# Performance work log

Hardware: AMD Instinct MI355X
Metric: run time of the kernel (lower is better)

Reference implementation:

```python
import jax, jax.numpy as jnp
import numpy as np

B, L, H, NH, NE, M = 4, 1024, 768, 12, 42, 8
EMB = 768
OFFSET = 1  # bert cls offset


def setup_inputs() -> dict:
    key = jax.random.key(0)
    ks = jax.random.split(key, 6)
    seq = jax.random.normal(ks[0], (B, L, H), jnp.float32)
    attn = jax.random.uniform(ks[1], (B, NH, L, L), jnp.float32)
    attn = attn / attn.sum(-1, keepdims=True)  # row-stochastic like softmaxed attention probs
    W_head = jax.random.normal(ks[2], (2 * H, EMB), jnp.float32) * 0.02
    b_head = jnp.zeros((EMB,), jnp.float32)
    W_tail = jax.random.normal(ks[3], (2 * H, EMB), jnp.float32) * 0.02
    b_tail = jnp.zeros((EMB,), jnp.float32)
    # mention start positions (before +offset); keep start+offset < L
    mention_pos = jax.random.randint(ks[4], (B, NE, M), 0, L - OFFSET - 1)
    counts = jax.random.randint(ks[5], (B, NE), 1, M + 1)  # >=1 valid mention per entity
    mention_mask = jnp.arange(M)[None, None, :] < counts[:, :, None]
    return dict(sequence_output=seq, attention=attn, W_head=W_head, b_head=b_head,
                W_tail=W_tail, b_tail=b_tail, mention_pos=mention_pos,
                mention_mask=mention_mask)


def _get_hrt(seq, attn, mention_pos, mention_mask):
    # seq: [B,L,H]; attn: [B,NH,L,L]; mention_pos/mask: [B,NE,M]
    b_idx = jnp.arange(B)[:, None, None]
    pos = mention_pos + OFFSET                          # [B,NE,M]
    m_emb = seq[b_idx, pos]                             # [B,NE,M,H] mention embeddings
    att_t = jnp.transpose(attn, (0, 2, 1, 3))           # [B,L,NH,L]
    m_att = att_t[b_idx, pos]                           # [B,NE,M,NH,L] mention attentions
    mask = mention_mask
    neg_inf = jnp.finfo(seq.dtype).min
    # per-entity logsumexp pooling over mentions
    ent_emb = jax.nn.logsumexp(jnp.where(mask[..., None], m_emb, neg_inf), axis=2)
    has_m = mask.any(axis=2)
    ent_emb = jnp.where(has_m[..., None], ent_emb, 0.0)  # [B,NE,H]
    cnt = mask.sum(axis=2).astype(seq.dtype)
    ent_att = (m_att * mask[..., None, None].astype(seq.dtype)).sum(axis=2)
    ent_att = ent_att / jnp.maximum(cnt, 1.0)[..., None, None]  # [B,NE,NH,L] mean over mentions
    # all ordered (head, tail) pairs on the NE x NE grid
    hs = jnp.broadcast_to(ent_emb[:, :, None, :], (B, NE, NE, H))
    ts = jnp.broadcast_to(ent_emb[:, None, :, :], (B, NE, NE, H))
    # ht_att = relu(mean_h(h_att * t_att)), normalized over seq, then context = ht_att @ seq
    ht = jnp.einsum('bihl,bjhl->bijl', ent_att, ent_att) / NH  # [B,NE,NE,L]
    ht = jax.nn.relu(ht)
    ht = ht / (ht.sum(-1, keepdims=True) + 1e-10)
    rs = jnp.einsum('bijl,bld->bijd', ht, seq)                  # [B,NE,NE,H]
    return hs, rs, ts


def reference(sequence_output, attention, W_head, b_head, W_tail, b_tail, mention_pos, mention_mask):
    hs, rs, ts = _get_hrt(sequence_output, attention, mention_pos, mention_mask)
    h_out = jnp.tanh(jnp.concatenate([hs, rs], axis=-1) @ W_head + b_head)
    t_out = jnp.tanh(jnp.concatenate([ts, rs], axis=-1) @ W_tail + b_tail)
    return h_out, t_out
```

## Files before the change

kernel.cpp:

```cpp
#include <hip/hip_runtime.h>
#include <math.h>

typedef _Float16 f16;
typedef __attribute__((ext_vector_type(4))) _Float16 f16x4;
typedef __attribute__((ext_vector_type(8))) _Float16 f16x8;
typedef __attribute__((ext_vector_type(4))) float f32x4;

#define B_    4
#define L_    1024
#define H_    768
#define NH_   12
#define NE_   42
#define M_    8
#define E2_   1536
#define HTP_  1792
#define OUT_HALF 5419008LL

typedef __attribute__((address_space(1))) const unsigned char ga_t;
typedef __attribute__((address_space(3))) unsigned char la_t;
__device__ __forceinline__ void async16(const void* g, void* l) {
    __builtin_amdgcn_global_load_lds((ga_t*)g, (la_t*)l, 16, 0, 0);
}

__device__ __forceinline__ float fast_tanh(float x) {
    float e = __expf(2.f * x);
    return 1.f - 2.f / (e + 1.f);
}


__device__ void prep_body(int bid, char* smem,
                          const float* __restrict__ Wh, const float* __restrict__ Wt,
                          const float* __restrict__ bh, const float* __restrict__ bt,
                          f16* __restrict__ wtop, f16* __restrict__ wbot,
                          float* __restrict__ bcat) {
    float (*tile)[33] = (float(*)[33])smem;
    int tx = bid % 24, ty = (bid / 24) % 24, m = bid / 576;
    const float* src = (m & 1) ? Wt : Wh;
    int roff = (m & 2) ? H_ : 0;
    f16* dst = (m & 2) ? wbot : wtop;
    int coff = (m & 1) ? H_ : 0;
    int x = threadIdx.x & 31, y8 = threadIdx.x >> 5;
#pragma unroll
    for (int r = 0; r < 4; r++) {
        int h = ty*32 + y8 + r*8, c = tx*32 + x;
        tile[y8 + r*8][x] = src[(long long)(roff + h)*H_ + c];
    }
    __syncthreads();
#pragma unroll
    for (int r = 0; r < 4; r++) {
        int c2 = tx*32 + y8 + r*8, h2 = ty*32 + x;
        dst[(long long)(coff + c2)*H_ + h2] = (f16)tile[x][y8 + r*8];
    }
    if (bid == 0) {
        for (int idx = threadIdx.x; idx < E2_; idx += 256)
            bcat[idx] = (idx < H_) ? bh[idx] : bt[idx - H_];
    }
}

__device__ void seq16_body(int bid, const float* __restrict__ seq,
                           f16* __restrict__ seq16) {
    int idx = (bid*256 + threadIdx.x) * 4;
    f32x4 v = *(const f32x4*)(seq + idx);
    f16x4 o = {(f16)v[0], (f16)v[1], (f16)v[2], (f16)v[3]};
    *(f16x4*)(seq16 + idx) = o;
}

__device__ void ent_emb_body(int bid, const float* __restrict__ seq,
                             const int* __restrict__ mpos,
                             const int* __restrict__ mmask,
                             f16* __restrict__ ent) {
    int e = bid % NE_, b = bid / NE_;
    int tid = threadIdx.x;
    const int* mp = mpos  + (b*NE_ + e)*M_;
    const int* mk = mmask + (b*NE_ + e)*M_;
    int pos[M_], msk[M_];
#pragma unroll
    for (int m = 0; m < M_; m++) { msk[m] = mk[m]; pos[m] = mp[m] + 1; }
#pragma unroll
    for (int q = 0; q < 3; q++) {
        int h = tid + q*256;
        float mx = -1e30f, vals[M_];
#pragma unroll
        for (int m = 0; m < M_; m++) {
            vals[m] = 0.f;
            if (msk[m]) {
                float v = seq[((long long)b*L_ + pos[m])*H_ + h];
                vals[m] = v; mx = fmaxf(mx, v);
            }
        }
        float s = 0.f;
#pragma unroll
        for (int m = 0; m < M_; m++) if (msk[m]) s += __expf(vals[m] - mx);
        float lse = (mx > -1e29f) ? mx + __logf(s) : 0.f;
        ent[(b*NE_ + e)*H_ + h] = (f16)lse;
    }
}

__device__ void ent_att_body(int bid, const float* __restrict__ attn,
                             const int* __restrict__ mpos,
                             const int* __restrict__ mmask,
                             f16* __restrict__ eatt) {
    int nh = bid % NH_, e = (bid / NH_) % NE_, b = bid / (NH_*NE_);
    int tid = threadIdx.x;
    int l0 = tid * 4;
    const int* mp = mpos  + (b*NE_ + e)*M_;
    const int* mk = mmask + (b*NE_ + e)*M_;
    const float* abase = attn + (long long)(b*NH_ + nh) * L_ * L_;
    f32x4 acc = {0,0,0,0}; int cnt = 0;
#pragma unroll
    for (int m = 0; m < M_; m++) {
        if (mk[m]) {
            cnt++;
            const float* row = abase + (long long)(mp[m] + 1) * L_;
            acc += *(const f32x4*)(row + l0);
        }
    }
    float inv = 1.f / (float)(cnt > 0 ? cnt : 1);
    f16x4 o = {(f16)(acc[0]*inv), (f16)(acc[1]*inv), (f16)(acc[2]*inv), (f16)(acc[3]*inv)};
    *(f16x4*)(eatt + ((long long)(b*NE_ + e)*NH_ + nh)*L_ + l0) = o;
}

__device__ void ht_body(int bid, char* smem, const f16* __restrict__ eatt,
                        f16* __restrict__ HT) {
    int jg = bid % 6, i = (bid / 6) % NE_, b = bid / 252;
    int tid = threadIdx.x;
    f16* ei_s = (f16*)smem;
    float (*red)[4] = (float(*)[4])(smem + NH_*L_*2);
    const f16* ei = eatt + (long long)(b*NE_ + i)*NH_*L_;
#pragma unroll
    for (int q = 0; q < 6; q++) {
        int off = (q*256 + tid)*8;
        *(f16x8*)(ei_s + off) = *(const f16x8*)(ei + off);
    }
    __syncthreads();
    int l0 = tid*4;
    int wave = tid >> 6, lane = tid & 63;
    for (int jj = 0; jj < 7; jj++) {
        int j = jg*7 + jj;
        const f16* ej = eatt + (long long)(b*NE_ + j)*NH_*L_;
        f32x4 acc = {0,0,0,0};
#pragma unroll
        for (int h = 0; h < NH_; h++) {
            f16x4 vi = *(const f16x4*)(ei_s + h*L_ + l0);
            f16x4 vj = *(const f16x4*)(ej   + h*L_ + l0);
#pragma unroll
            for (int r = 0; r < 4; r++) acc[r] += (float)vi[r] * (float)vj[r];
        }
        float v[4]; float s = 0.f;
#pragma unroll
        for (int r = 0; r < 4; r++) {
            float t = acc[r] * (1.f/12.f);
            t = t > 0.f ? t : 0.f;
            v[r] = t; s += t;
        }
#pragma unroll
        for (int m = 1; m < 64; m <<= 1) s += __shfl_xor(s, m, 64);
        if (lane == 0) red[jj][wave] = s;
        __syncthreads();
        float S = red[jj][0] + red[jj][1] + red[jj][2] + red[jj][3];
        float sc = 1.f / (S + 1e-10f);
        f16x4 o = {(f16)(v[0]*sc), (f16)(v[1]*sc), (f16)(v[2]*sc), (f16)(v[3]*sc)};
        *(f16x4*)(HT + ((long long)b*HTP_ + i*NE_ + j)*L_ + l0) = o;
    }
}

#define LDSS 40
__device__ void gemm_het_body(int bx, int by, char* smem,
                              const f16* __restrict__ A, const f16* __restrict__ BT,
                              float* __restrict__ het, const float* __restrict__ bcat) {
    const int M = 168, K = 768;
    f16* As = (f16*)smem;
    f16* Bs = (f16*)(smem + 64*LDSS*2);
    int bm = bx*64, bn = by*64;
    int tid = threadIdx.x;
    int wave = tid >> 6, lane = tid & 63;
    int wm = (wave >> 1)*32, wn = (wave & 1)*32;
    int lo4 = lane & 15, kq = (lane >> 4)*8;
    int srow = tid >> 2, scol = (tid & 3)*8;
    bool aval = (bm + srow) < M;
    const f16* aptr = A + (long long)(bm + srow)*K + scol;
    const f16* bptr = BT + (long long)(bn + srow)*K + scol;
    f32x4 acc[2][2] = {};
    for (int k0 = 0; k0 < K; k0 += 32) {
        uint4 zero = {0,0,0,0};
        uint4 av = aval ? *(const uint4*)(aptr + k0) : zero;
        uint4 bv = *(const uint4*)(bptr + k0);
        __syncthreads();
        *(uint4*)(As + srow*LDSS + scol) = av;
        *(uint4*)(Bs + srow*LDSS + scol) = bv;
        __syncthreads();
        f16x8 a0 = *(const f16x8*)(As + (wm +      lo4)*LDSS + kq);
        f16x8 a1 = *(const f16x8*)(As + (wm + 16 + lo4)*LDSS + kq);
        f16x8 b0 = *(const f16x8*)(Bs + (wn +      lo4)*LDSS + kq);
        f16x8 b1 = *(const f16x8*)(Bs + (wn + 16 + lo4)*LDSS + kq);
        acc[0][0] = __builtin_amdgcn_mfma_f32_16x16x32_f16(a0, b0, acc[0][0], 0,0,0);
        acc[0][1] = __builtin_amdgcn_mfma_f32_16x16x32_f16(a0, b1, acc[0][1], 0,0,0);
        acc[1][0] = __builtin_amdgcn_mfma_f32_16x16x32_f16(a1, b0, acc[1][0], 0,0,0);
        acc[1][1] = __builtin_amdgcn_mfma_f32_16x16x32_f16(a1, b1, acc[1][1], 0,0,0);
    }
    int rloc = (lane >> 4)*4;
#pragma unroll
    for (int sm = 0; sm < 2; sm++)
#pragma unroll
    for (int sn = 0; sn < 2; sn++) {
        f32x4 a = acc[sm][sn];
        int c  = bn + wn + sn*16 + lo4;
        int rb = bm + wm + sm*16 + rloc;
#pragma unroll
        for (int r = 0; r < 4; r++)
            if (rb + r < M) het[(rb + r)*E2_ + c] = a[r] + bcat[c];
    }
}

#define LDST 72
template<int MODE>
__device__ void gemm2_body(int bx, int by, int bz, char* smem,
                           const f16* __restrict__ A, const f16* __restrict__ BT, int K,
                           long long strideA, long long strideBT,
                           const float* __restrict__ het, float* __restrict__ outp,
                           f16* __restrict__ outp16) {
    f16* As = (f16*)smem;
    f16* Bs = (f16*)(smem + 8192);
    int bm = bx*128, bn = by*128;
    const f16* Ab = A + strideA*bz;
    const f16* Bb = BT + strideBT*bz;
    int tid = threadIdx.x, wave = tid >> 6, lane = tid & 63;
    int wm = (wave >> 1)*64, wn = (wave & 1)*64;
    int lo4 = lane & 15, kq = (lane >> 4)*8;
    int lrow = lane >> 2, lcol = (lane & 3)*8;
    const f16* ag = Ab + (long long)(bm + wave*32 + lrow)*K + lcol;
    const f16* bg = Bb + (long long)(bn + wave*32 + lrow)*K + lcol;
    f16* asl = As + wave*1024;
    f16* bsl = Bs + wave*1024;
    f32x4 acc[4][4] = {};
    for (int k0 = 0; k0 < K; k0 += 32) {
        async16(ag + k0,          asl);
        async16(ag + k0 + 16*K,   asl + 512);
        async16(bg + k0,          bsl);
        async16(bg + k0 + 16*K,   bsl + 512);
        __syncthreads();
        f16x8 af[4], bf[4];
#pragma unroll
        for (int s = 0; s < 4; s++) {
            af[s] = *(const f16x8*)(As + (wm + s*16 + lo4)*32 + kq);
            bf[s] = *(const f16x8*)(Bs + (wn + s*16 + lo4)*32 + kq);
        }
#pragma unroll
        for (int sm = 0; sm < 4; sm++)
#pragma unroll
        for (int sn = 0; sn < 4; sn++)
            acc[sm][sn] = __builtin_amdgcn_mfma_f32_16x16x32_f16(af[sm], bf[sn], acc[sm][sn], 0,0,0);
        __syncthreads();
    }
    int rloc = (lane >> 4)*4;
    if constexpr (MODE == 1) {
        f16* Ts = (f16*)smem;
        int h_of_wave = wave >> 1;
#pragma unroll
        for (int h = 0; h < 2; h++) {
            if (h_of_wave == h) {
#pragma unroll
                for (int sm = 0; sm < 4; sm++)
#pragma unroll
                for (int sn = 0; sn < 4; sn++) {
                    f32x4 a = acc[sm][sn];
                    int cl = wn + sn*16 + lo4;
                    int ll = sm*16 + rloc;
#pragma unroll
                    for (int r = 0; r < 4; r++)
                        Ts[cl*LDST + ll + r] = (f16)a[r];
                }
            }
            __syncthreads();
            {
                int cl = tid >> 1;
                int lb = (tid & 1)*32;
                f16* dst = outp16 + (long long)bz*E2_*L_
                         + (long long)(bn + cl)*L_ + bm + h*64 + lb;
                const f16* srcl = Ts + cl*LDST + lb;
#pragma unroll
                for (int q = 0; q < 4; q++)
                    *(f16x8*)(dst + q*8) = *(const f16x8*)(srcl + q*8);
            }
            __syncthreads();
        }
    } else {
#pragma unroll
        for (int sm = 0; sm < 4; sm++)
#pragma unroll
        for (int sn = 0; sn < 4; sn++) {
            f32x4 a = acc[sm][sn];
            int c  = bn + wn + sn*16 + lo4;
            int rb = bm + wm + sm*16 + rloc;
#pragma unroll
            for (int r = 0; r < 4; r++) {
                int row = rb + r;
                if (row < NE_*NE_) {
                    int i = row / NE_;
                    int j = row - i*NE_;
                    int sel = (c < H_) ? i : j;
                    float bias = het[(bz*NE_ + sel)*E2_ + c];
                    float v = fast_tanh(a[r] + bias);
                    long long o = (c < H_)
                        ? ((long long)((bz*NE_ + i)*NE_ + j))*H_ + c
                        : OUT_HALF + ((long long)((bz*NE_ + i)*NE_ + j))*H_ + (c - H_);
                    outp[o] = v;
                }
            }
        }
    }
}

__global__ __launch_bounds__(256) void k_L1(
        const float* __restrict__ seq, const float* __restrict__ attn,
        const float* __restrict__ Wh, const float* __restrict__ bh,
        const float* __restrict__ Wt, const float* __restrict__ bt,
        const int* __restrict__ mpos, const int* __restrict__ mmask,
        f16* __restrict__ wtop, f16* __restrict__ wbot, float* __restrict__ bcat,
        f16* __restrict__ seq16, f16* __restrict__ ent, f16* __restrict__ eatt) {
    __shared__ __align__(16) char smem[4224];
    int bid = blockIdx.x;
    if (bid < 2304)       prep_body(bid, smem, Wh, Wt, bh, bt, wtop, wbot, bcat);
    else if (bid < 5376)  seq16_body(bid - 2304, seq, seq16);
    else if (bid < 5544)  ent_emb_body(bid - 5376, seq, mpos, mmask, ent);
    else                  ent_att_body(bid - 5544, attn, mpos, mmask, eatt);
}

__global__ __launch_bounds__(256) void k_L2(
        const f16* __restrict__ seq16, const f16* __restrict__ wbot,
        const f16* __restrict__ ent, const f16* __restrict__ wtop,
        const float* __restrict__ bcat, const f16* __restrict__ eatt,
        f16* __restrict__ seqWT, float* __restrict__ het, f16* __restrict__ HT) {
    __shared__ __align__(16) char smem[24704];
    int bid = blockIdx.x;
    if (bid < 384) {
        int bx = bid & 7, by = (bid >> 3) % 12, bz = bid / 96;
        gemm2_body<1>(bx, by, bz, smem, seq16, wbot, 768,
                      (long long)L_*H_, 0, nullptr, nullptr, seqWT);
    } else if (bid < 1392) {
        ht_body(bid - 384, smem, eatt, HT);
    } else {
        int r = bid - 1392;
        gemm_het_body(r % 3, r / 3, smem, ent, wtop, het, bcat);
    }
}

__global__ __launch_bounds__(256) void k_L3(
        const f16* __restrict__ HT, const f16* __restrict__ seqWT,
        const float* __restrict__ het, float* __restrict__ outp) {
    __shared__ __align__(16) char smem[16384];
    int orig = blockIdx.x;
    int lid  = (orig & 7) * 84 + (orig >> 3);
    int bz   = lid / 168;
    int rem  = lid - bz*168;
    int bx   = rem / 12;
    int by   = rem - bx*12;
    gemm2_body<2>(bx, by, bz, smem, HT, seqWT, 1024,
                  (long long)HTP_*L_, (long long)E2_*L_, het, outp, nullptr);
}

extern "C" void kernel_launch(void* const* d_in, const int* in_sizes, int n_in,
                              void* d_out, int out_size, void* d_ws, size_t ws_size,
                              hipStream_t stream) {
    const float* seq  = (const float*)d_in[0];
    const float* attn = (const float*)d_in[1];
    const float* Wh   = (const float*)d_in[2];
    const float* bh   = (const float*)d_in[3];
    const float* Wt   = (const float*)d_in[4];
    const float* bt   = (const float*)d_in[5];
    const int* mpos   = (const int*)d_in[6];
    const int* mmask  = (const int*)d_in[7];
    float* out = (float*)d_out;
    char* ws = (char*)d_ws;
    f16*   ent   = (f16*)  (ws + 0);
    f16*   wtop  = (f16*)  (ws + 258048);
    f16*   wbot  = (f16*)  (ws + 2617344);
    float* bcat  = (float*)(ws + 4976640);
    float* het   = (float*)(ws + 4982784);
    f16*   eatt  = (f16*)  (ws + 6014976);
    f16*   seq16 = (f16*)  (ws + 10143744);
    f16*   HT    = (f16*)  (ws + 16435200);
    f16*   seqWT = (f16*)  (ws + 31115264);

    k_L1<<<7560, 256, 0, stream>>>(seq, attn, Wh, bh, Wt, bt, mpos, mmask,
                                   wtop, wbot, bcat, seq16, ent, eatt);
    k_L2<<<1464, 256, 0, stream>>>(seq16, wbot, ent, wtop, bcat, eatt,
                                   seqWT, het, HT);
    k_L3<<<672, 256, 0, stream>>>(HT, seqWT, het, out);
}
```

Measured before the change: 353.1 us.

## Double GEMM K-tile to 64 with XOR-swizzled LDS layout

The shared GEMM body now stages 64-wide K tiles instead of 32. Each thread issues four async 16-byte loads per operand, and each row of the LDS tile is XOR-swizzled so that fragment reads avoid bank conflicts. This halves the number of barrier pairs per K loop and raises the MFMA work done between syncs. In exchange, LDS use rises to 32 KB per block, which may reduce occupancy, and the loader addressing becomes more complex.

```diff
diff --git a/kernel.cpp b/kernel.cpp
--- a/kernel.cpp
+++ b/kernel.cpp
@@ -219,37 +219,51 @@
                            long long strideA, long long strideBT,
                            const float* __restrict__ het, float* __restrict__ outp,
                            f16* __restrict__ outp16) {
-    f16* As = (f16*)smem;
-    f16* Bs = (f16*)(smem + 8192);
+    char* As = smem;
+    char* Bs = smem + 16384;
     int bm = bx*128, bn = by*128;
     const f16* Ab = A + strideA*bz;
     const f16* Bb = BT + strideBT*bz;
     int tid = threadIdx.x, wave = tid >> 6, lane = tid & 63;
     int wm = (wave >> 1)*64, wn = (wave & 1)*64;
-    int lo4 = lane & 15, kq = (lane >> 4)*8;
-    int lrow = lane >> 2, lcol = (lane & 3)*8;
-    const f16* ag = Ab + (long long)(bm + wave*32 + lrow)*K + lcol;
-    const f16* bg = Bb + (long long)(bn + wave*32 + lrow)*K + lcol;
-    f16* asl = As + wave*1024;
-    f16* bsl = Bs + wave*1024;
+    int lo4 = lane & 15;
+    int kq2 = (lane >> 4)*16;
+    int sw  = (lo4 & 7) << 4;
+    int r0    = tid >> 3;
+    int scolb = ((tid & 7) * 16) ^ (((tid >> 3) & 7) << 4);
+    char* adst = As + (tid & ~63)*16;
+    char* bdst = Bs + (tid & ~63)*16;
+    const char* ag = (const char*)(Ab + (long long)(bm + r0)*K) + scolb;
+    const char* bg = (const char*)(Bb + (long long)(bn + r0)*K) + scolb;
+    long long rstep32 = (long long)32 * K * 2;
     f32x4 acc[4][4] = {};
-    for (int k0 = 0; k0 < K; k0 += 32) {
-        async16(ag + k0,          asl);
-        async16(ag + k0 + 16*K,   asl + 512);
-        async16(bg + k0,          bsl);
-        async16(bg + k0 + 16*K,   bsl + 512);
+    for (int k0 = 0; k0 < K; k0 += 64) {
+        long long kb = (long long)k0 * 2;
+#pragma unroll
+        for (int ld = 0; ld < 4; ld++)
+            async16(ag + kb + ld*rstep32, adst + ld*4096);
+#pragma unroll
+        for (int ld = 0; ld < 4; ld++)
+            async16(bg + kb + ld*rstep32, bdst + ld*4096);
         __syncthreads();
-        f16x8 af[4], bf[4];
+        f16x8 af[4][2], bf[4][2];
 #pragma unroll
         for (int s = 0; s < 4; s++) {
-            af[s] = *(const f16x8*)(As + (wm + s*16 + lo4)*32 + kq);
-            bf[s] = *(const f16x8*)(Bs + (wn + s*16 + lo4)*32 + kq);
+            char* pa = As + (wm + s*16 + lo4)*128;
+            char* pb = Bs + (wn + s*16 + lo4)*128;
+#pragma unroll
+            for (int kk = 0; kk < 2; kk++) {
+                af[s][kk] = *(const f16x8*)(pa + ((kk*64 + kq2) ^ sw));
+                bf[s][kk] = *(const f16x8*)(pb + ((kk*64 + kq2) ^ sw));
+            }
         }
 #pragma unroll
         for (int sm = 0; sm < 4; sm++)
 #pragma unroll
-        for (int sn = 0; sn < 4; sn++)
-            acc[sm][sn] = __builtin_amdgcn_mfma_f32_16x16x32_f16(af[sm], bf[sn], acc[sm][sn], 0,0,0);
+        for (int sn = 0; sn < 4; sn++) {
+            acc[sm][sn] = __builtin_amdgcn_mfma_f32_16x16x32_f16(af[sm][0], bf[sn][0], acc[sm][sn], 0,0,0);
+            acc[sm][sn] = __builtin_amdgcn_mfma_f32_16x16x32_f16(af[sm][1], bf[sn][1], acc[sm][sn], 0,0,0);
+        }
         __syncthreads();
     }
     int rloc = (lane >> 4)*4;
@@ -331,7 +345,7 @@
         const f16* __restrict__ ent, const f16* __restrict__ wtop,
         const float* __restrict__ bcat, const f16* __restrict__ eatt,
         f16* __restrict__ seqWT, float* __restrict__ het, f16* __restrict__ HT) {
-    __shared__ __align__(16) char smem[24704];
+    __shared__ __align__(16) char smem[32768];
     int bid = blockIdx.x;
     if (bid < 384) {
         int bx = bid & 7, by = (bid >> 3) % 12, bz = bid / 96;
@@ -348,7 +362,7 @@
 __global__ __launch_bounds__(256) void k_L3(
         const f16* __restrict__ HT, const f16* __restrict__ seqWT,
         const float* __restrict__ het, float* __restrict__ outp) {
-    __shared__ __align__(16) char smem[16384];
+    __shared__ __align__(16) char smem[32768];
     int orig = blockIdx.x;
     int lid  = (orig & 7) * 84 + (orig >> 3);
     int bz   = lid / 168;
```

Result: no change. 349.7 us (-1.0%).
